# Optimization experiments

Hardware: AMD Instinct MI355X
Metric: run time of the kernel (lower is better)

## Reference

```python
import jax, jax.numpy as jnp
import numpy as np

HIDDEN = 1024
FFN = 4096
NUM_EXPERTS = 8
TOP_K = 2
LOAD_BALANCE_WEIGHT = 0.01


def setup_inputs() -> dict:
    key = jax.random.key(0)
    ks = jax.random.split(key, 6)
    B, S = 4, 2048
    x = jax.random.normal(ks[0], (B, S, HIDDEN), dtype=jnp.float32)
    router_w = jax.random.normal(ks[1], (NUM_EXPERTS, HIDDEN), dtype=jnp.float32) * 0.02
    fc1_w = jax.random.normal(ks[2], (NUM_EXPERTS, FFN, HIDDEN), dtype=jnp.float32) * 0.02
    fc1_b = jnp.zeros((NUM_EXPERTS, FFN), dtype=jnp.float32)
    fc2_w = jax.random.normal(ks[3], (NUM_EXPERTS, HIDDEN, FFN), dtype=jnp.float32) * 0.02
    fc2_b = jnp.zeros((NUM_EXPERTS, HIDDEN), dtype=jnp.float32)
    return {"x": x, "router_w": router_w, "fc1_w": fc1_w, "fc1_b": fc1_b,
            "fc2_w": fc2_w, "fc2_b": fc2_b}


def reference(x, router_w, fc1_w, fc1_b, fc2_w, fc2_b):
    B, S, H = x.shape
    xf = x.reshape(-1, H)                       # [T, H]
    T = xf.shape[0]
    logits = xf @ router_w.T                    # [T, E]
    probs = jax.nn.softmax(logits, axis=-1)
    weights, indices = jax.lax.top_k(probs, TOP_K)   # [T, K]
    weights = weights / jnp.sum(weights, axis=-1, keepdims=True)
    # combine weight per (token, expert): sum of top-k weights assigned to expert
    onehot = jax.nn.one_hot(indices, NUM_EXPERTS, dtype=xf.dtype)  # [T, K, E]
    combine = jnp.sum(weights[..., None] * onehot, axis=1)          # [T, E]
    out = jnp.zeros_like(xf)
    for e in range(NUM_EXPERTS):
        h = jax.nn.gelu(xf @ fc1_w[e].T + fc1_b[e], approximate=False)
        y = h @ fc2_w[e].T + fc2_b[e]
        # tokens not routed to expert e have combine weight 0 -> contribute 0,
        # matching the torch masked gather/scatter-add exactly (dropout in eval).
        out = out + y * combine[:, e:e + 1]
    # load-balance aux loss
    counts = jnp.sum(onehot, axis=(0, 1))                # bincount of indices
    freq = counts / (T * TOP_K)
    aux_loss = LOAD_BALANCE_WEIGHT * NUM_EXPERTS * jnp.sum(jnp.mean(probs, axis=0) * freq)
    return out.reshape(B, S, H), aux_loss
```

## Files before the change

kernel.cpp:

```cpp
#include <hip/hip_runtime.h>
#include <math.h>

#define T_TOK 8192
#define HID 1024
#define FFN_DIM 4096
#define NEXP 8
#define BM 128
#define MAX_TILES 136

typedef __attribute__((ext_vector_type(8))) __bf16 bf16x8;
typedef __attribute__((ext_vector_type(8))) unsigned short ushort8;
typedef __attribute__((ext_vector_type(4))) float f32x4;

static __device__ __forceinline__ unsigned short f2bf(float f) {
  unsigned u = __builtin_bit_cast(unsigned, f);
  u += 0x7FFFu + ((u >> 16) & 1u);
  return (unsigned short)(u >> 16);
}

static __device__ __forceinline__ void gl16(const void* g, void* l) {
  __builtin_amdgcn_global_load_lds((const __attribute__((address_space(1))) unsigned int*)g,
                                   (__attribute__((address_space(3))) unsigned int*)l,
                                   16, 0, 0);
}

static __device__ __forceinline__ ushort8 cvt8(const float* p) {
  float4 a = *(const float4*)p, b = *(const float4*)(p + 4);
  ushort8 o;
  o[0] = f2bf(a.x); o[1] = f2bf(a.y); o[2] = f2bf(a.z); o[3] = f2bf(a.w);
  o[4] = f2bf(b.x); o[5] = f2bf(b.y); o[6] = f2bf(b.z); o[7] = f2bf(b.w);
  return o;
}

__global__ void moe_cvt_w(const float* __restrict__ w1, const float* __restrict__ w2,
                          unsigned short* __restrict__ w1b, unsigned short* __restrict__ w2b) {
  size_t i = ((size_t)blockIdx.x * 256 + threadIdx.x) * 8;
  if (blockIdx.y == 0) *(ushort8*)(w1b + i) = cvt8(w1 + i);
  else                 *(ushort8*)(w2b + i) = cvt8(w2 + i);
}

__global__ void moe_router(const float* __restrict__ x, const float* __restrict__ rw,
                           int* __restrict__ tok_idx, float* __restrict__ tok_w,
                           float* __restrict__ pbuf, unsigned short* __restrict__ xb) {
  int t = blockIdx.x * 4 + (threadIdx.x >> 6);
  int lane = threadIdx.x & 63;
  const float* xr = x + (size_t)t * HID;
  unsigned short* xbr = xb + (size_t)t * HID;
  double acc[NEXP];
#pragma unroll
  for (int e = 0; e < NEXP; ++e) acc[e] = 0.0;
  for (int i = 0; i < HID / 64; ++i) {
    float xv = xr[lane + 64 * i];
    xbr[lane + 64 * i] = f2bf(xv);
#pragma unroll
    for (int e = 0; e < NEXP; ++e)
      acc[e] += (double)xv * (double)rw[e * HID + lane + 64 * i];
  }
#pragma unroll
  for (int off = 32; off; off >>= 1)
#pragma unroll
    for (int e = 0; e < NEXP; ++e) acc[e] += __shfl_xor(acc[e], off);
  if (lane == 0) {
    double m = acc[0];
#pragma unroll
    for (int e = 1; e < NEXP; ++e) m = acc[e] > m ? acc[e] : m;
    float pf[NEXP], s = 0.0f;
#pragma unroll
    for (int e = 0; e < NEXP; ++e) { pf[e] = expf((float)(acc[e] - m)); s += pf[e]; }
    int i0 = 0;
#pragma unroll
    for (int e = 1; e < NEXP; ++e) if (acc[e] > acc[i0]) i0 = e;
    int i1 = (i0 == 0) ? 1 : 0;
#pragma unroll
    for (int e = 0; e < NEXP; ++e) if (e != i0 && acc[e] > acc[i1]) i1 = e;
    float w0 = pf[i0], w1 = pf[i1], wsum = w0 + w1;
    tok_idx[2 * t] = i0; tok_idx[2 * t + 1] = i1;
    tok_w[2 * t] = w0 / wsum; tok_w[2 * t + 1] = w1 / wsum;
    float inv = 1.0f / s;
#pragma unroll
    for (int e = 0; e < NEXP; ++e) pbuf[(size_t)t * NEXP + e] = pf[e] * inv;
  }
}

__global__ void moe_scatter(const int* __restrict__ tok_idx, const float* __restrict__ tok_w,
                            int* __restrict__ cursor, int* __restrict__ list,
                            float* __restrict__ listw) {
  const int e = blockIdx.x;
  __shared__ int wsum[16];
  __shared__ int base;
  const int tid = threadIdx.x, lane = tid & 63, wv = tid >> 6;
  if (tid == 0) base = 0;
  __syncthreads();
  for (int c = 0; c < 2 * T_TOK; c += 1024) {
    int i = c + tid;
    int m = (tok_idx[i] == e) ? 1 : 0;
    unsigned long long bal = __ballot(m);
    if (lane == 0) wsum[wv] = __popcll(bal);
    __syncthreads();
    int wbase = base;
    for (int k = 0; k < wv; ++k) wbase += wsum[k];
    if (m) {
      int pos = wbase + __popcll(bal & ((1ull << lane) - 1ull));
      list[e * T_TOK + pos] = i >> 1;
      listw[e * T_TOK + pos] = tok_w[i];
    }
    __syncthreads();
    if (tid == 0) {
      int s = 0;
#pragma unroll
      for (int k = 0; k < 16; ++k) s += wsum[k];
      base += s;
    }
    __syncthreads();
  }
  if (tid == 0) cursor[e] = base;
}

__global__ void moe_preduce(const float* __restrict__ pbuf, float* __restrict__ probs_sum) {
  const int e = blockIdx.x;
  float s = 0.0f;
  for (int t = threadIdx.x; t < T_TOK; t += 256) s += pbuf[(size_t)t * NEXP + e];
  __shared__ float red[4];
#pragma unroll
  for (int off = 32; off; off >>= 1) s += __shfl_down(s, off);
  if ((threadIdx.x & 63) == 0) red[threadIdx.x >> 6] = s;
  __syncthreads();
  if (threadIdx.x == 0) probs_sum[e] = red[0] + red[1] + red[2] + red[3];
}

__global__ void moe_offsets(const int* __restrict__ cursor, int* __restrict__ offs,
                            int* __restrict__ tile_e, int* __restrict__ tile_m,
                            int* __restrict__ meta) {
  if (threadIdx.x == 0 && blockIdx.x == 0) {
    int o = 0, t = 0;
    for (int e = 0; e < NEXP; ++e) {
      offs[e] = o;
      int ntl = (cursor[e] + BM - 1) / BM;
      for (int k = 0; k < ntl; ++k) { tile_e[t] = e; tile_m[t] = k; ++t; }
      o += ntl * BM;
    }
    offs[NEXP] = o;
    meta[0] = t;
  }
}

__global__ __launch_bounds__(256, 4) void moe_fc1(
    const unsigned short* __restrict__ xb, const unsigned short* __restrict__ w1b,
    const float* __restrict__ b1, const int* __restrict__ list,
    const int* __restrict__ offs, const int* __restrict__ tile_e,
    const int* __restrict__ tile_m, const int* __restrict__ meta,
    unsigned short* __restrict__ hbuf, int cb, int ch) {
  const int bid = blockIdx.x;
  const int c = bid & 7;
  const int k = bid >> 3;
  const int tl = c * 17 + k % 17;
  const int nt = k / 17;
  if (tl >= meta[0]) return;
  const int e = tile_e[tl], mt = tile_m[tl];
  __shared__ __align__(16) char As[BM * 128];
  __shared__ __align__(16) char Bs[BM * 128];
  const int tid = threadIdx.x, lane = tid & 63, wv = tid >> 6;
  const int wr = wv >> 1, wc = wv & 1;
  const int swz = ((lane & 7) ^ (lane >> 3)) << 4;
  const int rsub = lane >> 3;
  const int* le = list + e * T_TOK + mt * BM;
  const char* asrc[4]; const char* bsrc[4];
  char* adst[4]; char* bdst[4];
#pragma unroll
  for (int j = 0; j < 4; ++j) {
    int r = wv * 32 + j * 8 + rsub;
    int tok = le[r]; tok = tok < 0 ? 0 : tok;
    asrc[j] = (const char*)(xb + (size_t)tok * HID) + swz;
    bsrc[j] = (const char*)(w1b + ((size_t)e * FFN_DIM + cb + nt * BM + r) * HID) + swz;
    adst[j] = As + (wv * 32 + j * 8) * 128;
    bdst[j] = Bs + (wv * 32 + j * 8) * 128;
  }
  f32x4 acc[4][4] = {};
  for (int kt = 0; kt < 16; ++kt) {
    if (kt) __syncthreads();
#pragma unroll
    for (int j = 0; j < 4; ++j) {
      gl16(asrc[j] + kt * 128, adst[j]);
      gl16(bsrc[j] + kt * 128, bdst[j]);
    }
    __syncthreads();
#pragma unroll
    for (int kh = 0; kh < 2; ++kh) {
      bf16x8 afr[4], bfr[4];
      const int kb = kh * 64 + ((lane >> 4) << 4);
#pragma unroll
      for (int m = 0; m < 4; ++m) {
        int row = wr * 64 + m * 16 + (lane & 15);
        afr[m] = *(const bf16x8*)(As + row * 128 + (kb ^ ((row & 7) << 4)));
      }
#pragma unroll
      for (int n = 0; n < 4; ++n) {
        int col = wc * 64 + n * 16 + (lane & 15);
        bfr[n] = *(const bf16x8*)(Bs + col * 128 + (kb ^ ((col & 7) << 4)));
      }
#pragma unroll
      for (int m = 0; m < 4; ++m)
#pragma unroll
        for (int n = 0; n < 4; ++n)
          acc[m][n] = __builtin_amdgcn_mfma_f32_16x16x32_bf16(afr[m], bfr[n], acc[m][n], 0, 0, 0);
    }
  }
  const float* b1e = b1 + (size_t)e * FFN_DIM + cb + nt * BM;
  const size_t rbase = (size_t)(offs[e] + mt * BM);
#pragma unroll
  for (int n = 0; n < 4; ++n) {
    int cl = wc * 64 + n * 16 + (lane & 15);
    float bias = b1e[cl];
#pragma unroll
    for (int m = 0; m < 4; ++m)
#pragma unroll
      for (int j = 0; j < 4; ++j) {
        int rl = wr * 64 + m * 16 + ((lane >> 4) << 2) + j;
        float v = acc[m][n][j] + bias;
        float g = 0.5f * v * (1.0f + erff(v * 0.70710678118654752f));
        hbuf[(rbase + rl) * ch + nt * BM + cl] = f2bf(g);
      }
  }
}

__global__ __launch_bounds__(256, 4) void moe_fc2(
    const unsigned short* __restrict__ hbuf, const unsigned short* __restrict__ w2b,
    const float* __restrict__ b2, const int* __restrict__ list, const float* __restrict__ listw,
    const int* __restrict__ offs, const int* __restrict__ tile_e,
    const int* __restrict__ tile_m, const int* __restrict__ meta,
    float* __restrict__ out, int cb, int ch) {
  const int bid = blockIdx.x;
  const int c = bid & 7;
  const int k = bid >> 3;
  const int tl = c * 17 + (k >> 3);
  const int nt = k & 7;
  if (tl >= meta[0]) return;
  const int e = tile_e[tl], mt = tile_m[tl];
  const int nK = ch / 128;
  const int z = blockIdx.z;
  __shared__ __align__(16) char As[BM * 128];
  __shared__ __align__(16) char Bs[BM * 128];
  const int tid = threadIdx.x, lane = tid & 63, wv = tid >> 6;
  const int wr = wv >> 1, wc = wv & 1;
  const int swz = ((lane & 7) ^ (lane >> 3)) << 4;
  const int rsub = lane >> 3;
  const size_t rbase = (size_t)(offs[e] + mt * BM);
  const size_t koff = (size_t)z * nK * 128;
  const char* asrc[4]; const char* bsrc[4];
  char* adst[4]; char* bdst[4];
#pragma unroll
  for (int j = 0; j < 4; ++j) {
    int r = wv * 32 + j * 8 + rsub;
    asrc[j] = (const char*)(hbuf + (rbase + r) * ch) + koff + swz;
    bsrc[j] = (const char*)(w2b + ((size_t)e * HID + nt * BM + r) * FFN_DIM + cb) + koff + swz;
    adst[j] = As + (wv * 32 + j * 8) * 128;
    bdst[j] = Bs + (wv * 32 + j * 8) * 128;
  }
  f32x4 acc[4][4] = {};
  for (int kt = 0; kt < nK; ++kt) {
    if (kt) __syncthreads();
#pragma unroll
    for (int j = 0; j < 4; ++j) {
      gl16(asrc[j] + kt * 128, adst[j]);
      gl16(bsrc[j] + kt * 128, bdst[j]);
    }
    __syncthreads();
#pragma unroll
    for (int kh = 0; kh < 2; ++kh) {
      bf16x8 afr[4], bfr[4];
      const int kb = kh * 64 + ((lane >> 4) << 4);
#pragma unroll
      for (int m = 0; m < 4; ++m) {
        int row = wr * 64 + m * 16 + (lane & 15);
        afr[m] = *(const bf16x8*)(As + row * 128 + (kb ^ ((row & 7) << 4)));
      }
#pragma unroll
      for (int n = 0; n < 4; ++n) {
        int col = wc * 64 + n * 16 + (lane & 15);
        bfr[n] = *(const bf16x8*)(Bs + col * 128 + (kb ^ ((col & 7) << 4)));
      }
#pragma unroll
      for (int m = 0; m < 4; ++m)
#pragma unroll
        for (int n = 0; n < 4; ++n)
          acc[m][n] = __builtin_amdgcn_mfma_f32_16x16x32_bf16(afr[m], bfr[n], acc[m][n], 0, 0, 0);
    }
  }
  const int* le = list + e * T_TOK + mt * BM;
  const float* lw = listw + e * T_TOK + mt * BM;
  const float* b2e = b2 + (size_t)e * HID + nt * BM;
  const bool addb = (cb == 0) && (z == 0);
#pragma unroll
  for (int m = 0; m < 4; ++m)
#pragma unroll
    for (int j = 0; j < 4; ++j) {
      int rl = wr * 64 + m * 16 + ((lane >> 4) << 2) + j;
      int tok = le[rl];
      if (tok < 0) continue;
      float wgt = lw[rl];
      float* orow = out + (size_t)tok * HID + nt * BM;
#pragma unroll
      for (int n = 0; n < 4; ++n) {
        int cl = wc * 64 + n * 16 + (lane & 15);
        float v = acc[m][n][j];
        if (addb) v += b2e[cl];
        atomicAdd(orow + cl, wgt * v);
      }
    }
}

__global__ void moe_finalize(const float* __restrict__ probs_sum, const int* __restrict__ cursor,
                             float* __restrict__ out_aux) {
  if (threadIdx.x == 0 && blockIdx.x == 0) {
    float a = 0.0f;
    for (int e = 0; e < NEXP; ++e)
      a += (probs_sum[e] / (float)T_TOK) * ((float)cursor[e] / (float)(T_TOK * 2));
    out_aux[0] = 0.01f * (float)NEXP * a;
  }
}

extern "C" void kernel_launch(void* const* d_in, const int* in_sizes, int n_in,
                              void* d_out, int out_size, void* d_ws, size_t ws_size,
                              hipStream_t stream) {
  const float* x  = (const float*)d_in[0];
  const float* rw = (const float*)d_in[1];
  const float* w1 = (const float*)d_in[2];
  const float* b1 = (const float*)d_in[3];
  const float* w2 = (const float*)d_in[4];
  const float* b2 = (const float*)d_in[5];
  float* out = (float*)d_out;

  char* ws = (char*)d_ws;
  float* probs_sum = (float*)(ws + 0);
  int*   cursor    = (int*)(ws + 256);
  int*   meta      = (int*)(ws + 512);
  int*   offs      = (int*)(ws + 1024);
  int*   tile_e    = (int*)(ws + 2048);
  int*   tile_m    = (int*)(ws + 4096);
  int*   tok_idx   = (int*)(ws + 8192);
  float* tok_w     = (float*)(ws + 8192 + 65536);
  int*   list      = (int*)(ws + 8192 + 131072);
  float* listw     = (float*)(ws + 8192 + 393216);
  float* pbuf      = (float*)(ws + 8192 + 655360);
  unsigned short* xb   = (unsigned short*)(ws + 1048576);
  unsigned short* w1be = (unsigned short*)(ws + 17825792);
  unsigned short* w2be = (unsigned short*)(ws + 84934656);
  const size_t HBUF_OFF = 152043520;
  unsigned short* hbuf = (unsigned short*)(ws + HBUF_OFF);

  int CH = 4096;
  while (CH > 1024 && HBUF_OFF + (size_t)(MAX_TILES * BM) * CH * 2 > ws_size) CH >>= 1;

  hipMemsetAsync(d_out, 0, (size_t)out_size * sizeof(float), stream);
  hipMemsetAsync(ws + 8192 + 131072, 0xFF, 262144, stream);

  moe_cvt_w<<<dim3(16384, 2), 256, 0, stream>>>(w1, w2, w1be, w2be);
  moe_router<<<T_TOK / 4, 256, 0, stream>>>(x, rw, tok_idx, tok_w, pbuf, xb);
  moe_scatter<<<NEXP, 1024, 0, stream>>>(tok_idx, tok_w, cursor, list, listw);
  moe_preduce<<<NEXP, 256, 0, stream>>>(pbuf, probs_sum);
  moe_offsets<<<1, 1, 0, stream>>>(cursor, offs, tile_e, tile_m, meta);

  for (int cb = 0; cb < FFN_DIM; cb += CH) {
    moe_fc1<<<MAX_TILES * (CH / BM), 256, 0, stream>>>(
        xb, w1be, b1, list, offs, tile_e, tile_m, meta, hbuf, cb, CH);
    moe_fc2<<<dim3(MAX_TILES * 8, 1, 2), 256, 0, stream>>>(
        hbuf, w2be, b2, list, listw, offs, tile_e, tile_m, meta, out, cb, CH);
  }
  moe_finalize<<<1, 64, 0, stream>>>(probs_sum, cursor, out + (size_t)T_TOK * HID);
}
```

Baseline: 647.8 us.

## Triple-buffer LDS with async prefetch two stages ahead in MoE GEMMs

```diff
diff --git a/kernel.cpp b/kernel.cpp
--- a/kernel.cpp
+++ b/kernel.cpp
@@ -7,6 +7,7 @@
 #define NEXP 8
 #define BM 128
 #define MAX_TILES 136
+#define SLOTB 16384
 
 typedef __attribute__((ext_vector_type(8))) __bf16 bf16x8;
 typedef __attribute__((ext_vector_type(8))) unsigned short ushort8;
@@ -144,7 +145,16 @@
   }
 }
 
-__global__ __launch_bounds__(256, 4) void moe_fc1(
+#define PIPE_STAGE(Lbase, s, ktv)                                    \
+  {                                                                  \
+    char* Ld_ = (Lbase) + (s) * SLOTB + wv * 1024;                   \
+    gl16(aS0 + (size_t)(ktv) * 64, Ld_);                             \
+    gl16(aS1 + (size_t)(ktv) * 64, Ld_ + 4096);                      \
+    gl16(bS0 + (size_t)(ktv) * 64, Ld_ + 8192);                      \
+    gl16(bS1 + (size_t)(ktv) * 64, Ld_ + 12288);                     \
+  }
+
+__global__ __launch_bounds__(256, 3) void moe_fc1(
     const unsigned short* __restrict__ xb, const unsigned short* __restrict__ w1b,
     const float* __restrict__ b1, const int* __restrict__ list,
     const int* __restrict__ offs, const int* __restrict__ tile_e,
@@ -157,54 +167,60 @@
   const int nt = k / 17;
   if (tl >= meta[0]) return;
   const int e = tile_e[tl], mt = tile_m[tl];
-  __shared__ __align__(16) char As[BM * 128];
-  __shared__ __align__(16) char Bs[BM * 128];
+  __shared__ __align__(16) char L[3 * SLOTB];
   const int tid = threadIdx.x, lane = tid & 63, wv = tid >> 6;
   const int wr = wv >> 1, wc = wv & 1;
-  const int swz = ((lane & 7) ^ (lane >> 3)) << 4;
-  const int rsub = lane >> 3;
+  const int chunk = ((tid & 3) ^ ((tid >> 3) & 3)) << 4;
+  const int r0 = tid >> 2;
   const int* le = list + e * T_TOK + mt * BM;
-  const char* asrc[4]; const char* bsrc[4];
-  char* adst[4]; char* bdst[4];
-#pragma unroll
-  for (int j = 0; j < 4; ++j) {
-    int r = wv * 32 + j * 8 + rsub;
-    int tok = le[r]; tok = tok < 0 ? 0 : tok;
-    asrc[j] = (const char*)(xb + (size_t)tok * HID) + swz;
-    bsrc[j] = (const char*)(w1b + ((size_t)e * FFN_DIM + cb + nt * BM + r) * HID) + swz;
-    adst[j] = As + (wv * 32 + j * 8) * 128;
-    bdst[j] = Bs + (wv * 32 + j * 8) * 128;
-  }
+  int t0 = le[r0];       t0 = t0 < 0 ? 0 : t0;
+  int t1 = le[64 + r0];  t1 = t1 < 0 ? 0 : t1;
+  const char* aS0 = (const char*)(xb + (size_t)t0 * HID) + chunk;
+  const char* aS1 = (const char*)(xb + (size_t)t1 * HID) + chunk;
+  const char* bS0 = (const char*)(w1b + ((size_t)e * FFN_DIM + cb + nt * BM + r0) * HID) + chunk;
+  const char* bS1 = (const char*)(w1b + ((size_t)e * FFN_DIM + cb + nt * BM + 64 + r0) * HID) + chunk;
+
+  const int rsw = (((lane >> 4) ^ ((lane >> 1) & 3)) << 4);
+  const int ra = (wr * 64 + (lane & 15)) * 64;
+  const int rb = 8192 + (wc * 64 + (lane & 15)) * 64;
+
   f32x4 acc[4][4] = {};
-  for (int kt = 0; kt < 16; ++kt) {
-    if (kt) __syncthreads();
-#pragma unroll
-    for (int j = 0; j < 4; ++j) {
-      gl16(asrc[j] + kt * 128, adst[j]);
-      gl16(bsrc[j] + kt * 128, bdst[j]);
-    }
-    __syncthreads();
-#pragma unroll
-    for (int kh = 0; kh < 2; ++kh) {
-      bf16x8 afr[4], bfr[4];
-      const int kb = kh * 64 + ((lane >> 4) << 4);
-#pragma unroll
-      for (int m = 0; m < 4; ++m) {
-        int row = wr * 64 + m * 16 + (lane & 15);
-        afr[m] = *(const bf16x8*)(As + row * 128 + (kb ^ ((row & 7) << 4)));
-      }
-#pragma unroll
-      for (int n = 0; n < 4; ++n) {
-        int col = wc * 64 + n * 16 + (lane & 15);
-        bfr[n] = *(const bf16x8*)(Bs + col * 128 + (kb ^ ((col & 7) << 4)));
-      }
-#pragma unroll
-      for (int m = 0; m < 4; ++m)
-#pragma unroll
-        for (int n = 0; n < 4; ++n)
-          acc[m][n] = __builtin_amdgcn_mfma_f32_16x16x32_bf16(afr[m], bfr[n], acc[m][n], 0, 0, 0);
-    }
-  }
+  const int nK = HID / 32;
+
+  PIPE_STAGE(L, 0, 0);
+  PIPE_STAGE(L, 1, 1);
+  asm volatile("s_waitcnt vmcnt(4)" ::: "memory");
+  __builtin_amdgcn_s_barrier();
+  __builtin_amdgcn_sched_barrier(0);
+
+  int scur = 0, s2 = 2;
+  for (int kt = 0; kt < nK; ++kt) {
+    const char* Ab = L + scur * SLOTB;
+    bf16x8 afr[4], bfr[4];
+#pragma unroll
+    for (int m = 0; m < 4; ++m) afr[m] = *(const bf16x8*)(Ab + ra + m * 1024 + rsw);
+#pragma unroll
+    for (int n = 0; n < 4; ++n) bfr[n] = *(const bf16x8*)(Ab + rb + n * 1024 + rsw);
+    const bool stg = (kt + 2 < nK);
+    if (stg) PIPE_STAGE(L, s2, kt + 2);
+    __builtin_amdgcn_s_setprio(1);
+#pragma unroll
+    for (int m = 0; m < 4; ++m)
+#pragma unroll
+      for (int n = 0; n < 4; ++n)
+        acc[m][n] = __builtin_amdgcn_mfma_f32_16x16x32_bf16(afr[m], bfr[n], acc[m][n], 0, 0, 0);
+    __builtin_amdgcn_s_setprio(0);
+    if (stg) {
+      asm volatile("s_waitcnt vmcnt(4)" ::: "memory");
+    } else {
+      asm volatile("s_waitcnt vmcnt(0)" ::: "memory");
+    }
+    __builtin_amdgcn_s_barrier();
+    __builtin_amdgcn_sched_barrier(0);
+    scur = (scur == 2) ? 0 : scur + 1;
+    s2 = (s2 == 2) ? 0 : s2 + 1;
+  }
+
   const float* b1e = b1 + (size_t)e * FFN_DIM + cb + nt * BM;
   const size_t rbase = (size_t)(offs[e] + mt * BM);
 #pragma unroll
@@ -223,7 +239,7 @@
   }
 }
 
-__global__ __launch_bounds__(256, 4) void moe_fc2(
+__global__ __launch_bounds__(256, 3) void moe_fc2(
     const unsigned short* __restrict__ hbuf, const unsigned short* __restrict__ w2b,
     const float* __restrict__ b2, const int* __restrict__ list, const float* __restrict__ listw,
     const int* __restrict__ offs, const int* __restrict__ tile_e,
@@ -236,56 +252,60 @@
   const int nt = k & 7;
   if (tl >= meta[0]) return;
   const int e = tile_e[tl], mt = tile_m[tl];
-  const int nK = ch / 128;
   const int z = blockIdx.z;
-  __shared__ __align__(16) char As[BM * 128];
-  __shared__ __align__(16) char Bs[BM * 128];
+  __shared__ __align__(16) char L[3 * SLOTB];
   const int tid = threadIdx.x, lane = tid & 63, wv = tid >> 6;
   const int wr = wv >> 1, wc = wv & 1;
-  const int swz = ((lane & 7) ^ (lane >> 3)) << 4;
-  const int rsub = lane >> 3;
+  const int chunk = ((tid & 3) ^ ((tid >> 3) & 3)) << 4;
+  const int r0 = tid >> 2;
   const size_t rbase = (size_t)(offs[e] + mt * BM);
-  const size_t koff = (size_t)z * nK * 128;
-  const char* asrc[4]; const char* bsrc[4];
-  char* adst[4]; char* bdst[4];
-#pragma unroll
-  for (int j = 0; j < 4; ++j) {
-    int r = wv * 32 + j * 8 + rsub;
-    asrc[j] = (const char*)(hbuf + (rbase + r) * ch) + koff + swz;
-    bsrc[j] = (const char*)(w2b + ((size_t)e * HID + nt * BM + r) * FFN_DIM + cb) + koff + swz;
-    adst[j] = As + (wv * 32 + j * 8) * 128;
-    bdst[j] = Bs + (wv * 32 + j * 8) * 128;
-  }
+  const size_t koffb = (size_t)z * (ch / 2) * 2;
+  const char* aS0 = (const char*)(hbuf + (rbase + r0) * ch) + koffb + chunk;
+  const char* aS1 = (const char*)(hbuf + (rbase + 64 + r0) * ch) + koffb + chunk;
+  const char* bS0 = (const char*)(w2b + ((size_t)e * HID + nt * BM + r0) * FFN_DIM + cb) + koffb + chunk;
+  const char* bS1 = (const char*)(w2b + ((size_t)e * HID + nt * BM + 64 + r0) * FFN_DIM + cb) + koffb + chunk;
+
+  const int rsw = (((lane >> 4) ^ ((lane >> 1) & 3)) << 4);
+  const int ra = (wr * 64 + (lane & 15)) * 64;
+  const int rb = 8192 + (wc * 64 + (lane & 15)) * 64;
+
   f32x4 acc[4][4] = {};
+  const int nK = (ch / 2) / 32;
+
+  PIPE_STAGE(L, 0, 0);
+  PIPE_STAGE(L, 1, 1);
+  asm volatile("s_waitcnt vmcnt(4)" ::: "memory");
+  __builtin_amdgcn_s_barrier();
+  __builtin_amdgcn_sched_barrier(0);
+
+  int scur = 0, s2 = 2;
   for (int kt = 0; kt < nK; ++kt) {
-    if (kt) __syncthreads();
-#pragma unroll
-    for (int j = 0; j < 4; ++j) {
-      gl16(asrc[j] + kt * 128, adst[j]);
-      gl16(bsrc[j] + kt * 128, bdst[j]);
-    }
-    __syncthreads();
-#pragma unroll
-    for (int kh = 0; kh < 2; ++kh) {
-      bf16x8 afr[4], bfr[4];
-      const int kb = kh * 64 + ((lane >> 4) << 4);
-#pragma unroll
-      for (int m = 0; m < 4; ++m) {
-        int row = wr * 64 + m * 16 + (lane & 15);
-        afr[m] = *(const bf16x8*)(As + row * 128 + (kb ^ ((row & 7) << 4)));
-      }
-#pragma unroll
-      for (int n = 0; n < 4; ++n) {
-        int col = wc * 64 + n * 16 + (lane & 15);
-        bfr[n] = *(const bf16x8*)(Bs + col * 128 + (kb ^ ((col & 7) << 4)));
-      }
-#pragma unroll
-      for (int m = 0; m < 4; ++m)
-#pragma unroll
-        for (int n = 0; n < 4; ++n)
-          acc[m][n] = __builtin_amdgcn_mfma_f32_16x16x32_bf16(afr[m], bfr[n], acc[m][n], 0, 0, 0);
-    }
-  }
+    const char* Ab = L + scur * SLOTB;
+    bf16x8 afr[4], bfr[4];
+#pragma unroll
+    for (int m = 0; m < 4; ++m) afr[m] = *(const bf16x8*)(Ab + ra + m * 1024 + rsw);
+#pragma unroll
+    for (int n = 0; n < 4; ++n) bfr[n] = *(const bf16x8*)(Ab + rb + n * 1024 + rsw);
+    const bool stg = (kt + 2 < nK);
+    if (stg) PIPE_STAGE(L, s2, kt + 2);
+    __builtin_amdgcn_s_setprio(1);
+#pragma unroll
+    for (int m = 0; m < 4; ++m)
+#pragma unroll
+      for (int n = 0; n < 4; ++n)
+        acc[m][n] = __builtin_amdgcn_mfma_f32_16x16x32_bf16(afr[m], bfr[n], acc[m][n], 0, 0, 0);
+    __builtin_amdgcn_s_setprio(0);
+    if (stg) {
+      asm volatile("s_waitcnt vmcnt(4)" ::: "memory");
+    } else {
+      asm volatile("s_waitcnt vmcnt(0)" ::: "memory");
+    }
+    __builtin_amdgcn_s_barrier();
+    __builtin_amdgcn_sched_barrier(0);
+    scur = (scur == 2) ? 0 : scur + 1;
+    s2 = (s2 == 2) ? 0 : s2 + 1;
+  }
+
   const int* le = list + e * T_TOK + mt * BM;
   const float* lw = listw + e * T_TOK + mt * BM;
   const float* b2e = b2 + (size_t)e * HID + nt * BM;
```

New measurement: 664.9 us. 2.6% more time.
